# Kernel optimization log

Hardware: AMD Instinct MI355X
Metric: run time of the kernel (lower is better)

The kernel has to match this reference:

```python
import jax, jax.numpy as jnp
import numpy as np

B, T, N = 8, 168, 1024
FD, FS, FF = 16, 32, 8
DL, DG, HE, E = 128, 128, 4, 16384
BN = B * N


def _lstm_last(x, Wih, Whh, bih, bhh):
    # x: (BN, T, FD); PyTorch gate order i, f, g, o
    h0 = jnp.zeros((x.shape[0], Whh.shape[1]), x.dtype)
    def step(carry, xt):
        h, c = carry
        g = xt @ Wih.T + h @ Whh.T + bih + bhh
        i, f, gg, o = jnp.split(g, 4, axis=-1)
        c = jax.nn.sigmoid(f) * c + jax.nn.sigmoid(i) * jnp.tanh(gg)
        h = jax.nn.sigmoid(o) * jnp.tanh(c)
        return (h, c), None
    (h, _), _ = jax.lax.scan(step, (h0, h0), jnp.swapaxes(x, 0, 1))
    return h


def _ln(x, g, b):
    mu = x.mean(-1, keepdims=True)
    v = ((x - mu) ** 2).mean(-1, keepdims=True)
    return (x - mu) / jnp.sqrt(v + 1e-5) * g + b


def _gat(x, src, dst, ea, W, a_src, a_dst, a_edge, We, bias):
    # PyG GATConv: concat=False (mean over heads), edge_dim=1, LeakyReLU(0.2)
    xl = (x @ W.T).reshape(BN, HE, -1)                 # (BN, H, C)
    as_ = jnp.sum(xl * a_src, -1)                      # (BN, H)
    ad_ = jnp.sum(xl * a_dst, -1)
    ep = (ea @ We.T).reshape(-1, HE, xl.shape[-1])     # (Eb, H, C)
    ae_ = jnp.sum(ep * a_edge, -1)                     # (Eb, H)
    alpha = jax.nn.leaky_relu(as_[src] + ad_[dst] + ae_, 0.2)
    amax = jax.ops.segment_max(alpha, dst, num_segments=BN)
    ex = jnp.exp(alpha - amax[dst])
    den = jax.ops.segment_sum(ex, dst, num_segments=BN)
    w = ex / den[dst]                                  # softmax over incoming edges
    out = jax.ops.segment_sum(w[:, :, None] * xl[src], dst, num_segments=BN)
    return out.mean(axis=1) + bias


def _forward(fl, edge_index):
    (dyn, fcst, sta, ew,
     lWih, lWhh, lbih, lbhh, sW, sb, fW, fb, uW, ub,
     g0W, g0as, g0ad, g0ae, g0We, g0b,
     g1W, g1as, g1ad, g1ae, g1We, g1b,
     n0g, n0b, n1g, n1b, oW, ob) = fl
    x = jnp.transpose(dyn, (0, 2, 1, 3)).reshape(BN, T, FD)
    z = _lstm_last(x, lWih, lWhh, lbih, lbhh)
    s = jax.nn.relu(sta.reshape(BN, -1) @ sW.T + sb)
    f = jax.nn.relu(fcst.reshape(BN, -1) @ fW.T + fb)
    h = jax.nn.relu(jnp.concatenate([z, s, f], -1) @ uW.T + ub)
    # batch the graph: B disjoint copies with node offsets
    off = (jnp.arange(B) * N)[:, None]
    src = (edge_index[0][None] + off).reshape(-1)
    dst = (edge_index[1][None] + off).reshape(-1)
    ea = jnp.tile(ew.reshape(-1, 1), (B, 1))           # (B*E, 1)
    # PyG GATConv default add_self_loops=True, fill_value='mean' of incoming edge attrs
    deg = jax.ops.segment_sum(jnp.ones_like(ea), dst, num_segments=BN)
    loop_ea = jax.ops.segment_sum(ea, dst, num_segments=BN) / jnp.maximum(deg, 1.0)
    loops = jnp.arange(BN)
    src = jnp.concatenate([src, loops])
    dst = jnp.concatenate([dst, loops])
    ea = jnp.concatenate([ea, loop_ea], 0)
    # hop 0: relu on delta (not last hop), residual (res_proj=None since DL==DG), LayerNorm
    d0 = jax.nn.relu(_gat(h, src, dst, ea, g0W, g0as, g0ad, g0ae, g0We, g0b))
    h = _ln(h + d0, n0g, n0b)
    # hop 1: last hop, no relu on delta
    d1 = _gat(h, src, dst, ea, g1W, g1as, g1ad, g1ae, g1We, g1b)
    h = _ln(h + d1, n1g, n1b)
    return (h @ oW.T + ob).reshape(B, N)


def setup_inputs():
    key = jax.random.key(0)
    ks = iter(jax.random.split(key, 48))
    def rn(shape, s=0.08):
        return jax.random.normal(next(ks), shape, jnp.float32) * s
    HO = HE * DG  # heads * out_channels
    return dict(
        dynamic_features=rn((B, T, N, FD), 1.0),
        forecast_features=rn((B, N, FF), 1.0),
        static_features=rn((B, N, FS), 1.0),
        edge_index=jax.random.randint(next(ks), (2, E), 0, N),
        edge_weight=jax.random.uniform(next(ks), (E,), jnp.float32),
        lstm_Wih=rn((4 * DL, FD)), lstm_Whh=rn((4 * DL, DL)),
        lstm_bih=rn((4 * DL,)), lstm_bhh=rn((4 * DL,)),
        static_W=rn((DL, FS)), static_b=rn((DL,)),
        fcst_W=rn((DL, FF)), fcst_b=rn((DL,)),
        fusion_W=rn((DL, 3 * DL)), fusion_b=rn((DL,)),
        gat0_W=rn((HO, DL)), gat0_att_src=rn((1, HE, DG)), gat0_att_dst=rn((1, HE, DG)),
        gat0_att_edge=rn((1, HE, DG)), gat0_We=rn((HO, 1)), gat0_bias=rn((DG,)),
        gat1_W=rn((HO, DG)), gat1_att_src=rn((1, HE, DG)), gat1_att_dst=rn((1, HE, DG)),
        gat1_att_edge=rn((1, HE, DG)), gat1_We=rn((HO, 1)), gat1_bias=rn((DG,)),
        ln0_g=jnp.ones((DG,), jnp.float32), ln0_b=jnp.zeros((DG,), jnp.float32),
        ln1_g=jnp.ones((DG,), jnp.float32), ln1_b=jnp.zeros((DG,), jnp.float32),
        out_W=rn((1, DG)), out_b=rn((1,)),
    )


def reference(dynamic_features, forecast_features, static_features, edge_weight,
              lstm_Wih, lstm_Whh, lstm_bih, lstm_bhh, static_W, static_b,
              fcst_W, fcst_b, fusion_W, fusion_b,
              gat0_W, gat0_att_src, gat0_att_dst, gat0_att_edge, gat0_We, gat0_bias,
              gat1_W, gat1_att_src, gat1_att_dst, gat1_att_edge, gat1_We, gat1_bias,
              ln0_g, ln0_b, ln1_g, ln1_b, out_W, out_b, edge_index):
    fl = (dynamic_features, forecast_features, static_features, edge_weight,
          lstm_Wih, lstm_Whh, lstm_bih, lstm_bhh, static_W, static_b,
          fcst_W, fcst_b, fusion_W, fusion_b,
          gat0_W, gat0_att_src, gat0_att_dst, gat0_att_edge, gat0_We, gat0_bias,
          gat1_W, gat1_att_src, gat1_att_dst, gat1_att_edge, gat1_We, gat1_bias,
          ln0_g, ln0_b, ln1_g, ln1_b, out_W, out_b)
    return _forward(fl, edge_index)
```

## Files before the change

### kernel.cpp

```cpp
#include <hip/hip_runtime.h>
#include <hip/hip_bf16.h>
#include <stdint.h>

#define BB 8
#define TT 168
#define NN 1024
#define BN_ 8192
#define FD_ 16
#define EE 16384

typedef short short8 __attribute__((ext_vector_type(8)));
typedef __bf16 bf16x8 __attribute__((ext_vector_type(8)));
typedef float f32x4 __attribute__((ext_vector_type(4)));

#if __has_builtin(__builtin_amdgcn_exp2f)
#define EXP2(x) __builtin_amdgcn_exp2f(x)
#else
#define EXP2(x) exp2f(x)
#endif
#if __has_builtin(__builtin_amdgcn_rcpf)
#define RCPF(x) __builtin_amdgcn_rcpf(x)
#else
#define RCPF(x) (1.f / (x))
#endif
#define L2E 1.4426950408889634f
#define T2E 2.8853900817779268f

static __device__ __forceinline__ float b2f(ushort s) {
    unsigned u = ((unsigned)s) << 16;
    return __builtin_bit_cast(float, u);
}
static __device__ __forceinline__ ushort f2b(float f) {
    unsigned u = __builtin_bit_cast(unsigned, f);
    unsigned lsb = (u >> 16) & 1u;
    u += 0x7fffu + lsb;
    return (ushort)(u >> 16);
}
static __device__ __forceinline__ ushort f2b_fast(float f) {
    unsigned u = __builtin_bit_cast(unsigned, f);
    return (ushort)((u + 0x8000u) >> 16);
}
static __device__ __forceinline__ f32x4 mfma16(short8 a, short8 b, f32x4 c) {
    return __builtin_amdgcn_mfma_f32_16x16x32_bf16(
        __builtin_bit_cast(bf16x8, a), __builtin_bit_cast(bf16x8, b), c, 0, 0, 0);
}

#define O_WIH 0
#define O_WHH 8192
#define O_STA 73728
#define O_FCS 335872
#define O_SW  401408
#define O_FW  405504
#define O_UW  406528
#define O_G0W 455680
#define O_G1W 521216
#define O_END 586752

__global__ void cast_kernel(const float* __restrict__ Wih, const float* __restrict__ Whh,
                            const float* __restrict__ sta, const float* __restrict__ fcst,
                            const float* __restrict__ sW, const float* __restrict__ fW,
                            const float* __restrict__ uW, const float* __restrict__ g0W,
                            const float* __restrict__ g1W, ushort* __restrict__ dst) {
    const int i = blockIdx.x * 256 + threadIdx.x;
    if (i >= O_END) return;
    float v;
    if      (i < O_WHH) v = Wih[i - O_WIH];
    else if (i < O_STA) v = Whh[i - O_WHH];
    else if (i < O_FCS) v = sta[i - O_STA];
    else if (i < O_SW)  v = fcst[i - O_FCS];
    else if (i < O_FW)  v = sW[i - O_SW];
    else if (i < O_UW)  v = fW[i - O_FW];
    else if (i < O_G0W) v = uW[i - O_UW];
    else if (i < O_G1W) v = g0W[i - O_G0W];
    else                v = g1W[i - O_G1W];
    dst[i] = f2b(v);
}

__global__ __launch_bounds__(1024) void prep_kernel(
    const int* __restrict__ ei, const float* __restrict__ ew,
    const float* __restrict__ We0, const float* __restrict__ ae0,
    const float* __restrict__ We1, const float* __restrict__ ae1,
    int* __restrict__ deg0, int* __restrict__ offs, float* __restrict__ loopea,
    int* __restrict__ eidx, float* __restrict__ se) {
    __shared__ int degL[1024];
    __shared__ float wsL[1024];
    __shared__ int sc[1024];
    __shared__ float seL[8];
    const int t = threadIdx.x;
    degL[t] = 0; wsL[t] = 0.f;
    if (t < 8) seL[t] = 0.f;
    __syncthreads();
    for (int e = t; e < EE; e += 1024) {
        const int d = ei[EE + e];
        atomicAdd(&degL[d], 1);
        atomicAdd(&wsL[d], ew[e]);
    }
    __syncthreads();
    const int d = degL[t];
    sc[t] = d;
    __syncthreads();
    for (int o = 1; o < 1024; o <<= 1) {
        const int v = (t >= o) ? sc[t - o] : 0;
        __syncthreads();
        sc[t] += v;
        __syncthreads();
    }
    const int excl = sc[t] - d;
    offs[t] = excl;
    deg0[t] = d;
    loopea[t] = wsL[t] / fmaxf((float)d, 1.f);
    degL[t] = excl;
    __syncthreads();
    for (int e = t; e < EE; e += 1024) {
        const int dd = ei[EE + e];
        const int slot = atomicAdd(&degL[dd], 1);
        eidx[slot] = e;
    }
    const int g = t >> 7, k = t & 127;
    const int head = g & 3;
    const float* W = (g >> 2) ? We1 : We0;
    const float* A = (g >> 2) ? ae1 : ae0;
    atomicAdd(&seL[g], W[head * 128 + k] * A[head * 128 + k]);
    __syncthreads();
    if (t < 8) se[t] = seL[t];
}

__global__ __launch_bounds__(256, 2) void lstm_kernel(
    const float* __restrict__ dyn,
    const ushort* __restrict__ Wih,
    const ushort* __restrict__ Whh,
    const float* __restrict__ bih,
    const float* __restrict__ bhh,
    ushort* __restrict__ zsf)
{
    constexpr int HS = 168;
    __shared__ ushort hbuf[2][16 * HS];

    const int tid = threadIdx.x;
    const int blk = blockIdx.x;
    const int b = blk >> 6;
    const int n0 = (blk & 63) << 4;
    const int w = tid >> 6, lane = tid & 63, quad = lane >> 4, m = lane & 15;

    short8 Bf[5][4][2];
    float ci[2], cf[2], cg[2], co[2];
#pragma unroll
    for (int jj = 0; jj < 2; jj++) {
        const int u = (2 * w + jj) * 16 + m;
#pragma unroll
        for (int g = 0; g < 4; g++) {
            const int grow = g * 128 + u;
#pragma unroll
            for (int kt = 0; kt < 4; kt++)
                Bf[kt][g][jj] = *(const short8*)(Whh + grow * 128 + kt * 32 + quad * 8);
            if (quad < 2) Bf[4][g][jj] = *(const short8*)(Wih + grow * 16 + quad * 8);
            else          Bf[4][g][jj] = short8{0, 0, 0, 0, 0, 0, 0, 0};
        }
        ci[jj] = -L2E * (bih[u] + bhh[u]);
        cf[jj] = -L2E * (bih[128 + u] + bhh[128 + u]);
        cg[jj] =  T2E * (bih[256 + u] + bhh[256 + u]);
        co[jj] = -L2E * (bih[384 + u] + bhh[384 + u]);
    }

    float c[2][4];
#pragma unroll
    for (int jj = 0; jj < 2; jj++)
#pragma unroll
        for (int r = 0; r < 4; r++) c[jj][r] = 0.f;

    for (int i = tid; i < 2 * 16 * HS; i += 256) ((ushort*)hbuf)[i] = 0;
    __syncthreads();

    const int xn = tid >> 4, xf = tid & 15;
    const size_t xbase = (size_t)b * TT * NN * FD_ + (size_t)(n0 + xn) * FD_ + xf;
    hbuf[0][xn * HS + 128 + xf] = f2b(dyn[xbase]);
    float xv = dyn[xbase + (size_t)NN * FD_];
    __syncthreads();

    for (int t = 0; t < TT; t++) {
        const ushort* rb = hbuf[t & 1];
        ushort* wb = hbuf[(t + 1) & 1];
        if (t + 1 < TT) wb[xn * HS + 128 + xf] = f2b(xv);
        if (t + 2 < TT) xv = dyn[xbase + (size_t)(t + 2) * NN * FD_];

        f32x4 acc[4][2];
#pragma unroll
        for (int g = 0; g < 4; g++)
#pragma unroll
            for (int jj = 0; jj < 2; jj++) acc[g][jj] = f32x4{0.f, 0.f, 0.f, 0.f};
#pragma unroll
        for (int kt = 0; kt < 5; kt++) {
            short8 a = *(const short8*)&rb[m * HS + kt * 32 + quad * 8];
#pragma unroll
            for (int g = 0; g < 4; g++)
#pragma unroll
                for (int jj = 0; jj < 2; jj++)
                    acc[g][jj] = mfma16(a, Bf[kt][g][jj], acc[g][jj]);
        }

#pragma unroll
        for (int jj = 0; jj < 2; jj++) {
            const int u = (2 * w + jj) * 16 + m;
#pragma unroll
            for (int r = 0; r < 4; r++) {
                const int n = quad * 4 + r;
                const float Di = 1.f + EXP2(fmaf(acc[0][jj][r], -L2E, ci[jj]));
                const float Df = 1.f + EXP2(fmaf(acc[1][jj][r], -L2E, cf[jj]));
                const float Eg = EXP2(fmaf(acc[2][jj][r], T2E, cg[jj]));
                const float Do = 1.f + EXP2(fmaf(acc[3][jj][r], -L2E, co[jj]));
                const float R  = RCPF(Di * (1.f + Eg));
                const float sf = RCPF(Df);
                const float cc = fmaf(sf, c[jj][r], (Eg - 1.f) * R);
                c[jj][r] = cc;
                const float Ec = EXP2(T2E * cc);
                const float h = (Ec - 1.f) * RCPF(Do * (1.f + Ec));
                wb[n * HS + u] = f2b_fast(h);
                if (t == TT - 1) zsf[(size_t)(blk * 16 + n) * 384 + u] = f2b_fast(h);
            }
        }
        __syncthreads();
    }
}

__global__ __launch_bounds__(256) void gemm_sf_kernel(
    const ushort* __restrict__ staB, const ushort* __restrict__ sWB,
    const float* __restrict__ sb,
    const ushort* __restrict__ fcsB, const ushort* __restrict__ fWB,
    const float* __restrict__ fb, ushort* __restrict__ zsf) {
    const int tid = threadIdx.x;
    const int lane = tid & 63, quad = lane >> 4, m = lane & 15;
    int wave = blockIdx.x * 4 + (tid >> 6);
    const short8 z8 = short8{0, 0, 0, 0, 0, 0, 0, 0};
    short8 a, bf;
    int r0, c0, ocol;
    const float* bias;
    if (wave < 4096) {
        r0 = (wave >> 3) * 16; c0 = (wave & 7) * 16; ocol = 128; bias = sb;
        a  = *(const short8*)(staB + (size_t)(r0 + m) * 32 + quad * 8);
        bf = *(const short8*)(sWB + (size_t)(c0 + m) * 32 + quad * 8);
    } else {
        wave -= 4096;
        r0 = (wave >> 3) * 16; c0 = (wave & 7) * 16; ocol = 256; bias = fb;
        a  = (quad == 0) ? *(const short8*)(fcsB + (size_t)(r0 + m) * 8) : z8;
        bf = (quad == 0) ? *(const short8*)(fWB + (size_t)(c0 + m) * 8) : z8;
    }
    f32x4 acc = mfma16(a, bf, f32x4{0.f, 0.f, 0.f, 0.f});
    const float bv = bias[c0 + m];
#pragma unroll
    for (int r = 0; r < 4; r++) {
        const int row = r0 + quad * 4 + r;
        zsf[(size_t)row * 384 + ocol + c0 + m] = f2b(fmaxf(acc[r] + bv, 0.f));
    }
}

__global__ __launch_bounds__(256) void gemm_fusion_kernel(
    const ushort* __restrict__ A, const ushort* __restrict__ Bt,
    const float* __restrict__ bias, ushort* __restrict__ hB, float* __restrict__ hF) {
    const int tid = threadIdx.x;
    const int lane = tid & 63, quad = lane >> 4, m = lane & 15;
    const int wave = blockIdx.x * 4 + (tid >> 6);
    const int r0 = (wave >> 3) * 16, c0 = (wave & 7) * 16;
    f32x4 acc = f32x4{0.f, 0.f, 0.f, 0.f};
#pragma unroll
    for (int kt = 0; kt < 12; kt++) {
        const int k = kt * 32 + quad * 8;
        short8 a  = *(const short8*)(A + (size_t)(r0 + m) * 384 + k);
        short8 bf = *(const short8*)(Bt + (size_t)(c0 + m) * 384 + k);
        acc = mfma16(a, bf, acc);
    }
    const int col = c0 + m;
    const float bv = bias[col];
#pragma unroll
    for (int r = 0; r < 4; r++) {
        const int row = r0 + quad * 4 + r;
        const float v = fmaxf(acc[r] + bv, 0.f);
        hB[(size_t)row * 128 + col] = f2b(v);
        hF[(size_t)row * 128 + col] = v;
    }
}

__global__ __launch_bounds__(256) void gemmatt_kernel(
    const ushort* __restrict__ hB, const ushort* __restrict__ W,
    const float* __restrict__ asrc, const float* __restrict__ adst,
    ushort* __restrict__ xl, float* __restrict__ as_, float* __restrict__ ad_) {
    const int tid = threadIdx.x;
    const int lane = tid & 63, quad = lane >> 4, m = lane & 15;
    const int w = tid >> 6;
    const int r0 = blockIdx.x * 16;
    f32x4 acc[8];
#pragma unroll
    for (int ct = 0; ct < 8; ct++) acc[ct] = f32x4{0.f, 0.f, 0.f, 0.f};
#pragma unroll
    for (int kt = 0; kt < 4; kt++) {
        const int k = kt * 32 + quad * 8;
        short8 a = *(const short8*)(hB + (size_t)(r0 + m) * 128 + k);
#pragma unroll
        for (int ct = 0; ct < 8; ct++) {
            short8 bf = *(const short8*)(W + (size_t)(w * 128 + ct * 16 + m) * 128 + k);
            acc[ct] = mfma16(a, bf, acc[ct]);
        }
    }
    float sa[4] = {0.f, 0.f, 0.f, 0.f}, sd[4] = {0.f, 0.f, 0.f, 0.f};
#pragma unroll
    for (int ct = 0; ct < 8; ct++) {
        const int col = w * 128 + ct * 16 + m;
        const float av = asrc[col], dv = adst[col];
#pragma unroll
        for (int r = 0; r < 4; r++) {
            const float v = acc[ct][r];
            xl[(size_t)(r0 + quad * 4 + r) * 512 + col] = f2b(v);
            sa[r] = fmaf(v, av, sa[r]);
            sd[r] = fmaf(v, dv, sd[r]);
        }
    }
#pragma unroll
    for (int o = 1; o < 16; o <<= 1) {
#pragma unroll
        for (int r = 0; r < 4; r++) {
            sa[r] += __shfl_xor(sa[r], o);
            sd[r] += __shfl_xor(sd[r], o);
        }
    }
    if (m == 0) {
#pragma unroll
        for (int r = 0; r < 4; r++) {
            const int node = r0 + quad * 4 + r;
            as_[node * 4 + w] = sa[r];
            ad_[node * 4 + w] = sd[r];
        }
    }
}

__global__ __launch_bounds__(256) void edge_exp_kernel(
    const int* __restrict__ ei, const float* __restrict__ ew,
    const float* __restrict__ as_, const float* __restrict__ ad_,
    const float* __restrict__ se4, float* __restrict__ pexp) {
    const int idx = blockIdx.x * 256 + threadIdx.x;
    const int b = idx >> 14, e = idx & (EE - 1);
    const int src = b * 1024 + ei[e];
    const int dst = b * 1024 + ei[EE + e];
    const float eaw = ew[e];
    const float4 s4 = *(const float4*)(as_ + src * 4);
    const float4 d4 = *(const float4*)(ad_ + dst * 4);
    float4 p;
    float* pp = (float*)&p;
    const float* s = (const float*)&s4;
    const float* d = (const float*)&d4;
#pragma unroll
    for (int h = 0; h < 4; h++) {
        float a = s[h] + d[h] + eaw * se4[h];
        a = (a < 0.f) ? 0.2f * a : a;
        pp[h] = EXP2(fminf(a, 60.f) * L2E);
    }
    *(float4*)(pexp + (size_t)idx * 4) = p;
}

__global__ __launch_bounds__(256) void gat_kernel(
    float* __restrict__ hF, ushort* __restrict__ hB, const ushort* __restrict__ xl,
    const float* __restrict__ as_, const float* __restrict__ ad_,
    const float* __restrict__ pexp,
    const int* __restrict__ eidx, const int* __restrict__ offs,
    const int* __restrict__ deg0, const float* __restrict__ loopea,
    const int* __restrict__ ei,
    const float* __restrict__ se4, const float* __restrict__ bias,
    const float* __restrict__ lng, const float* __restrict__ lnb, int relu,
    int writeOut, const float* __restrict__ oW, const float* __restrict__ ob,
    float* __restrict__ out) {
    const int lane = threadIdx.x & 63;
    const int v = blockIdx.x * 4 + (threadIdx.x >> 6);
    const int b = v >> 10, n = v & 1023;
    const int dg = deg0[n], off = offs[n];

    const float lea = loopea[n];
    const float4 s4 = *(const float4*)(as_ + v * 4);
    const float4 d4 = *(const float4*)(ad_ + v * 4);
    const float* sp = (const float*)&s4;
    const float* dp = (const float*)&d4;
    float den[4], num0[4], num1[4];
#pragma unroll
    for (int h = 0; h < 4; h++) {
        float a = sp[h] + dp[h] + lea * se4[h];
        a = (a < 0.f) ? 0.2f * a : a;
        const float p = EXP2(fminf(a, 60.f) * L2E);
        den[h] = p;
        num0[h] = p * b2f(xl[(size_t)v * 512 + h * 128 + lane]);
        num1[h] = p * b2f(xl[(size_t)v * 512 + h * 128 + 64 + lane]);
    }
    for (int i = 0; i < dg; i++) {
        const int e = eidx[off + i];
        const int src = b * 1024 + ei[e];
        const float4 p4 = *(const float4*)(pexp + (size_t)(b * EE + e) * 4);
        const float* p = (const float*)&p4;
        const ushort* xr = xl + (size_t)src * 512;
#pragma unroll
        for (int h = 0; h < 4; h++) {
            den[h] += p[h];
            num0[h] = fmaf(p[h], b2f(xr[h * 128 + lane]), num0[h]);
            num1[h] = fmaf(p[h], b2f(xr[h * 128 + 64 + lane]), num1[h]);
        }
    }
    float o0 = 0.f, o1 = 0.f;
#pragma unroll
    for (int h = 0; h < 4; h++) {
        const float inv = RCPF(den[h]);
        o0 = fmaf(num0[h], inv, o0);
        o1 = fmaf(num1[h], inv, o1);
    }

    float d0 = o0 * 0.25f + bias[lane];
    float d1 = o1 * 0.25f + bias[64 + lane];
    if (relu) { d0 = fmaxf(d0, 0.f); d1 = fmaxf(d1, 0.f); }
    const float x0 = hF[(size_t)v * 128 + lane] + d0;
    const float x1 = hF[(size_t)v * 128 + 64 + lane] + d1;

    float s = x0 + x1;
#pragma unroll
    for (int o = 32; o; o >>= 1) s += __shfl_xor(s, o);
    const float mu = s * (1.f / 128.f);
    const float e0 = x0 - mu, e1 = x1 - mu;
    float vs = e0 * e0 + e1 * e1;
#pragma unroll
    for (int o = 32; o; o >>= 1) vs += __shfl_xor(vs, o);
    const float r = rsqrtf(vs * (1.f / 128.f) + 1e-5f);
    const float y0 = e0 * r * lng[lane] + lnb[lane];
    const float y1 = e1 * r * lng[64 + lane] + lnb[64 + lane];
    if (writeOut) {
        float t = y0 * oW[lane] + y1 * oW[64 + lane];
#pragma unroll
        for (int o = 32; o; o >>= 1) t += __shfl_xor(t, o);
        if (lane == 0) out[v] = t + ob[0];
    } else {
        hF[(size_t)v * 128 + lane] = y0;
        hF[(size_t)v * 128 + 64 + lane] = y1;
        hB[(size_t)v * 128 + lane] = f2b(y0);
        hB[(size_t)v * 128 + 64 + lane] = f2b(y1);
    }
}

extern "C" void kernel_launch(void* const* d_in, const int* in_sizes, int n_in,
                              void* d_out, int out_size, void* d_ws, size_t ws_size,
                              hipStream_t stream) {
    const float* dyn  = (const float*)d_in[0];
    const float* fcst = (const float*)d_in[1];
    const float* sta  = (const float*)d_in[2];
    const int*   ei   = (const int*)d_in[3];
    const float* ew   = (const float*)d_in[4];
    const float* lWih = (const float*)d_in[5];
    const float* lWhh = (const float*)d_in[6];
    const float* lbih = (const float*)d_in[7];
    const float* lbhh = (const float*)d_in[8];
    const float* sW = (const float*)d_in[9];
    const float* sb = (const float*)d_in[10];
    const float* fW = (const float*)d_in[11];
    const float* fb = (const float*)d_in[12];
    const float* uW = (const float*)d_in[13];
    const float* ub = (const float*)d_in[14];
    const float* g0W  = (const float*)d_in[15];
    const float* g0as = (const float*)d_in[16];
    const float* g0ad = (const float*)d_in[17];
    const float* g0ae = (const float*)d_in[18];
    const float* g0We = (const float*)d_in[19];
    const float* g0b  = (const float*)d_in[20];
    const float* g1W  = (const float*)d_in[21];
    const float* g1as = (const float*)d_in[22];
    const float* g1ad = (const float*)d_in[23];
    const float* g1ae = (const float*)d_in[24];
    const float* g1We = (const float*)d_in[25];
    const float* g1b  = (const float*)d_in[26];
    const float* ln0g = (const float*)d_in[27];
    const float* ln0b = (const float*)d_in[28];
    const float* ln1g = (const float*)d_in[29];
    const float* ln1b = (const float*)d_in[30];
    const float* oW = (const float*)d_in[31];
    const float* ob = (const float*)d_in[32];

    char* p = (char*)d_ws;
    ushort* castB = (ushort*)p; p += (size_t)O_END * 2 + 512;
    ushort* zsf = (ushort*)p;  p += (size_t)BN_ * 384 * 2;
    float*  hF  = (float*)p;   p += (size_t)BN_ * 128 * 4;
    ushort* hB  = (ushort*)p;  p += (size_t)BN_ * 128 * 2;
    ushort* xl  = (ushort*)p;  p += (size_t)BN_ * 512 * 2;
    float*  asb = (float*)p;   p += (size_t)BN_ * 4 * 4;
    float*  adb = (float*)p;   p += (size_t)BN_ * 4 * 4;
    int*    deg0   = (int*)p;   p += 4096;
    int*    offs   = (int*)p;   p += 4096;
    float*  loopea = (float*)p; p += 4096;
    int*    eidx   = (int*)p;   p += (size_t)EE * 4;
    float*  se     = (float*)p; p += 256;
    float*  pexp   = (float*)zsf;

    const ushort* WihB = castB + O_WIH;
    const ushort* WhhB = castB + O_WHH;
    const ushort* staB = castB + O_STA;
    const ushort* fcsB = castB + O_FCS;
    const ushort* sWB  = castB + O_SW;
    const ushort* fWB  = castB + O_FW;
    const ushort* uWB  = castB + O_UW;
    const ushort* g0WB = castB + O_G0W;
    const ushort* g1WB = castB + O_G1W;

    cast_kernel<<<(O_END + 255) / 256, 256, 0, stream>>>(lWih, lWhh, sta, fcst, sW, fW,
                                                         uW, g0W, g1W, castB);
    prep_kernel<<<1, 1024, 0, stream>>>(ei, ew, g0We, g0ae, g1We, g1ae,
                                        deg0, offs, loopea, eidx, se);

    lstm_kernel<<<512, 256, 0, stream>>>(dyn, WihB, WhhB, lbih, lbhh, zsf);
    gemm_sf_kernel<<<2048, 256, 0, stream>>>(staB, sWB, sb, fcsB, fWB, fb, zsf);
    gemm_fusion_kernel<<<1024, 256, 0, stream>>>(zsf, uWB, ub, hB, hF);

    gemmatt_kernel<<<512, 256, 0, stream>>>(hB, g0WB, g0as, g0ad, xl, asb, adb);
    edge_exp_kernel<<<512, 256, 0, stream>>>(ei, ew, asb, adb, se, pexp);
    gat_kernel<<<2048, 256, 0, stream>>>(hF, hB, xl, asb, adb, pexp, eidx, offs, deg0,
                                         loopea, ei, se, g0b, ln0g, ln0b, 1,
                                         0, oW, ob, (float*)d_out);
    gemmatt_kernel<<<512, 256, 0, stream>>>(hB, g1WB, g1as, g1ad, xl, asb, adb);
    edge_exp_kernel<<<512, 256, 0, stream>>>(ei, ew, asb, adb, se + 4, pexp);
    gat_kernel<<<2048, 256, 0, stream>>>(hF, hB, xl, asb, adb, pexp, eidx, offs, deg0,
                                         loopea, ei, se + 4, g1b, ln1g, ln1b, 0,
                                         1, oW, ob, (float*)d_out);
}
```

Baseline: 574.5 us.

## Split LSTM hidden units across eight waves and merge gate reciprocals

The LSTM block grows from 4 to 8 waves, each owning one 16-unit column tile instead of two. This halves per-thread MFMA work and register-resident weights per timestep, so the serial recurrence has more parallelism. The cell update is also rewritten algebraically so the input and forget gate reciprocals share a single rcp. The cost is twice as many threads contending at the per-step __syncthreads, plus slightly different floating-point rounding.

```diff
diff --git a/kernel.cpp b/kernel.cpp
--- a/kernel.cpp
+++ b/kernel.cpp
@@ -125,7 +125,7 @@
     if (t < 8) se[t] = seL[t];
 }
 
-__global__ __launch_bounds__(256, 2) void lstm_kernel(
+__global__ __launch_bounds__(512, 4) void lstm_kernel(
     const float* __restrict__ dyn,
     const ushort* __restrict__ Wih,
     const ushort* __restrict__ Whh,
@@ -142,81 +142,74 @@
     const int n0 = (blk & 63) << 4;
     const int w = tid >> 6, lane = tid & 63, quad = lane >> 4, m = lane & 15;
 
-    short8 Bf[5][4][2];
-    float ci[2], cf[2], cg[2], co[2];
-#pragma unroll
-    for (int jj = 0; jj < 2; jj++) {
-        const int u = (2 * w + jj) * 16 + m;
-#pragma unroll
-        for (int g = 0; g < 4; g++) {
-            const int grow = g * 128 + u;
-#pragma unroll
-            for (int kt = 0; kt < 4; kt++)
-                Bf[kt][g][jj] = *(const short8*)(Whh + grow * 128 + kt * 32 + quad * 8);
-            if (quad < 2) Bf[4][g][jj] = *(const short8*)(Wih + grow * 16 + quad * 8);
-            else          Bf[4][g][jj] = short8{0, 0, 0, 0, 0, 0, 0, 0};
-        }
-        ci[jj] = -L2E * (bih[u] + bhh[u]);
-        cf[jj] = -L2E * (bih[128 + u] + bhh[128 + u]);
-        cg[jj] =  T2E * (bih[256 + u] + bhh[256 + u]);
-        co[jj] = -L2E * (bih[384 + u] + bhh[384 + u]);
-    }
-
-    float c[2][4];
-#pragma unroll
-    for (int jj = 0; jj < 2; jj++)
-#pragma unroll
-        for (int r = 0; r < 4; r++) c[jj][r] = 0.f;
-
-    for (int i = tid; i < 2 * 16 * HS; i += 256) ((ushort*)hbuf)[i] = 0;
-    __syncthreads();
-
-    const int xn = tid >> 4, xf = tid & 15;
+    short8 Bf[5][4];
+    const int u = w * 16 + m;
+#pragma unroll
+    for (int g = 0; g < 4; g++) {
+        const int grow = g * 128 + u;
+#pragma unroll
+        for (int kt = 0; kt < 4; kt++)
+            Bf[kt][g] = *(const short8*)(Whh + grow * 128 + kt * 32 + quad * 8);
+        if (quad < 2) Bf[4][g] = *(const short8*)(Wih + grow * 16 + quad * 8);
+        else          Bf[4][g] = short8{0, 0, 0, 0, 0, 0, 0, 0};
+    }
+    const float ci = -L2E * (bih[u] + bhh[u]);
+    const float cf = -L2E * (bih[128 + u] + bhh[128 + u]);
+    const float cg =  T2E * (bih[256 + u] + bhh[256 + u]);
+    const float co = -L2E * (bih[384 + u] + bhh[384 + u]);
+
+    float c[4] = {0.f, 0.f, 0.f, 0.f};
+
+    for (int i = tid; i < 2 * 16 * HS; i += 512) ((ushort*)hbuf)[i] = 0;
+    __syncthreads();
+
+    const int xn = (tid >> 4) & 15, xf = tid & 15;
     const size_t xbase = (size_t)b * TT * NN * FD_ + (size_t)(n0 + xn) * FD_ + xf;
-    hbuf[0][xn * HS + 128 + xf] = f2b(dyn[xbase]);
-    float xv = dyn[xbase + (size_t)NN * FD_];
+    float xv = 0.f;
+    if (tid < 256) {
+        hbuf[0][xn * HS + 128 + xf] = f2b(dyn[xbase]);
+        xv = dyn[xbase + (size_t)NN * FD_];
+    }
     __syncthreads();
 
     for (int t = 0; t < TT; t++) {
         const ushort* rb = hbuf[t & 1];
         ushort* wb = hbuf[(t + 1) & 1];
-        if (t + 1 < TT) wb[xn * HS + 128 + xf] = f2b(xv);
-        if (t + 2 < TT) xv = dyn[xbase + (size_t)(t + 2) * NN * FD_];
-
-        f32x4 acc[4][2];
-#pragma unroll
-        for (int g = 0; g < 4; g++)
-#pragma unroll
-            for (int jj = 0; jj < 2; jj++) acc[g][jj] = f32x4{0.f, 0.f, 0.f, 0.f};
+        if (tid < 256) {
+            if (t + 1 < TT) wb[xn * HS + 128 + xf] = f2b(xv);
+            if (t + 2 < TT) xv = dyn[xbase + (size_t)(t + 2) * NN * FD_];
+        }
+
+        f32x4 acc[4];
+#pragma unroll
+        for (int g = 0; g < 4; g++) acc[g] = f32x4{0.f, 0.f, 0.f, 0.f};
 #pragma unroll
         for (int kt = 0; kt < 5; kt++) {
             short8 a = *(const short8*)&rb[m * HS + kt * 32 + quad * 8];
 #pragma unroll
             for (int g = 0; g < 4; g++)
-#pragma unroll
-                for (int jj = 0; jj < 2; jj++)
-                    acc[g][jj] = mfma16(a, Bf[kt][g][jj], acc[g][jj]);
-        }
-
-#pragma unroll
-        for (int jj = 0; jj < 2; jj++) {
-            const int u = (2 * w + jj) * 16 + m;
-#pragma unroll
-            for (int r = 0; r < 4; r++) {
-                const int n = quad * 4 + r;
-                const float Di = 1.f + EXP2(fmaf(acc[0][jj][r], -L2E, ci[jj]));
-                const float Df = 1.f + EXP2(fmaf(acc[1][jj][r], -L2E, cf[jj]));
-                const float Eg = EXP2(fmaf(acc[2][jj][r], T2E, cg[jj]));
-                const float Do = 1.f + EXP2(fmaf(acc[3][jj][r], -L2E, co[jj]));
-                const float R  = RCPF(Di * (1.f + Eg));
-                const float sf = RCPF(Df);
-                const float cc = fmaf(sf, c[jj][r], (Eg - 1.f) * R);
-                c[jj][r] = cc;
-                const float Ec = EXP2(T2E * cc);
-                const float h = (Ec - 1.f) * RCPF(Do * (1.f + Ec));
-                wb[n * HS + u] = f2b_fast(h);
-                if (t == TT - 1) zsf[(size_t)(blk * 16 + n) * 384 + u] = f2b_fast(h);
-            }
+                acc[g] = mfma16(a, Bf[kt][g], acc[g]);
+        }
+
+#pragma unroll
+        for (int r = 0; r < 4; r++) {
+            const int n = quad * 4 + r;
+            const float ei = EXP2(fmaf(acc[0][r], -L2E, ci));
+            const float ef = EXP2(fmaf(acc[1][r], -L2E, cf));
+            const float Eg = EXP2(fmaf(acc[2][r],  T2E, cg));
+            const float eo = EXP2(fmaf(acc[3][r], -L2E, co));
+            const float G1 = 1.f + Eg;
+            const float P  = fmaf(ei, G1, G1);
+            const float Df = 1.f + ef;
+            const float num = fmaf(c[r], P, (Eg - 1.f) * Df);
+            const float cn = num * RCPF(Df * P);
+            c[r] = cn;
+            const float Ec = EXP2(T2E * cn);
+            const float C1 = 1.f + Ec;
+            const float Po = fmaf(eo, C1, C1);
+            const float h = (Ec - 1.f) * RCPF(Po);
+            wb[n * HS + u] = f2b_fast(h);
+            if (t == TT - 1) zsf[(size_t)(blk * 16 + n) * 384 + u] = f2b_fast(h);
         }
         __syncthreads();
     }
@@ -504,7 +497,7 @@
     prep_kernel<<<1, 1024, 0, stream>>>(ei, ew, g0We, g0ae, g1We, g1ae,
                                         deg0, offs, loopea, eidx, se);
 
-    lstm_kernel<<<512, 256, 0, stream>>>(dyn, WihB, WhhB, lbih, lbhh, zsf);
+    lstm_kernel<<<512, 512, 0, stream>>>(dyn, WihB, WhhB, lbih, lbhh, zsf);
     gemm_sf_kernel<<<2048, 256, 0, stream>>>(staB, sWB, sb, fcsB, fWB, fb, zsf);
     gemm_fusion_kernel<<<1024, 256, 0, stream>>>(zsf, uWB, ub, hB, hF);
 
```

After: 578.0 us. No clear change (+0.6%).
